# Optimization experiments

Measured on AMD Instinct MI355X. Metric: run time of the kernel, lower is better.

## Reference

```python
import jax, jax.numpy as jnp
import numpy as np

N = 50000       # nodes
E = 800000      # edges
F_IN = 128      # num_node_features
H = 128         # hidden_channels
C = 10          # num_classes
G = 512         # graphs in batch


def _glorot(key, shape):
    fan_in, fan_out = shape
    lim = float(np.sqrt(6.0 / (fan_in + fan_out)))
    return jax.random.uniform(key, shape, jnp.float32, -lim, lim)


def setup_inputs() -> dict:
    key = jax.random.key(0)
    ks = jax.random.split(key, 12)
    x = jax.random.normal(ks[0], (N, F_IN), jnp.float32)
    edge_index = jax.random.randint(ks[1], (2, E), 0, N, dtype=jnp.int32).astype(jnp.int64)
    batch = jnp.sort(jax.random.randint(ks[2], (N,), 0, G, dtype=jnp.int32)).astype(jnp.int64)
    return {
        "x": x,
        "edge_index": edge_index,
        "batch": batch,
        "W1": _glorot(ks[3], (F_IN, H)), "b1": jnp.zeros((H,), jnp.float32),
        "W2": _glorot(ks[4], (H, H)),    "b2": jnp.zeros((H,), jnp.float32),
        "W3": _glorot(ks[5], (H, H)),    "b3": jnp.zeros((H,), jnp.float32),
        "W_lin": _glorot(ks[6], (H, C)), "b_lin": jnp.zeros((C,), jnp.float32),
    }


def _gcn_conv(h_in, W, b, src, dst, dis):
    # GCNConv: D^{-1/2} (A + I) D^{-1/2} (X W) + b  (symmetric norm, self-loops)
    h = h_in @ W                                   # [N, H]
    coef = (dis[src] * dis[dst])[:, None]          # [E, 1]
    msg = h[src] * coef                            # gather + scale
    agg = jax.ops.segment_sum(msg, dst, num_segments=N)  # scatter-add at targets
    agg = agg + h * (dis * dis)[:, None]           # self-loop term
    return agg + b


def reference(x, edge_index, batch, W1, b1, W2, b2, W3, b3, W_lin, b_lin):
    src, dst = edge_index[0], edge_index[1]
    # degree with self-loops (counted at aggregation target, PyG convention)
    deg = jax.ops.segment_sum(jnp.ones((E,), jnp.float32), dst, num_segments=N) + 1.0
    dis = jax.lax.rsqrt(deg)

    h = jax.nn.relu(_gcn_conv(x, W1, b1, src, dst, dis))
    h = jax.nn.relu(_gcn_conv(h, W2, b2, src, dst, dis))
    h = _gcn_conv(h, W3, b3, src, dst, dis)

    # global mean pool over graphs
    counts = jax.ops.segment_sum(jnp.ones((N,), jnp.float32), batch, num_segments=G)
    pooled = jax.ops.segment_sum(h, batch, num_segments=G)
    pooled = pooled / jnp.maximum(counts, 1.0)[:, None]

    # dropout(p=0.5, training=False) -> identity
    return pooled @ W_lin + b_lin
```

## Files before the change

kernel.cpp:

```cpp
#include <hip/hip_runtime.h>

#define NN 50000
#define NE 800000
#define FD 128
#define NG 512
#define NC 10

#define NBUCK 98
#define BSHIFT 9
#define BSTRIDE 10240
#define P1_EPB 4096
#define P1_BLOCKS ((NE + P1_EPB - 1) / P1_EPB)

typedef __attribute__((ext_vector_type(8))) short bf16x8;
typedef __attribute__((ext_vector_type(4))) float f32x4;


__device__ __forceinline__ float bf2f(unsigned short u) {
  return __uint_as_float(((unsigned int)u) << 16);
}
__device__ __forceinline__ unsigned short f2bf(float f) {
  unsigned int b = __float_as_uint(f);
  b += 0x7FFF + ((b >> 16) & 1);
  return (unsigned short)(b >> 16);
}


__global__ __launch_bounds__(128) void init_kernel(int* __restrict__ gcursor) {
  int i = threadIdx.x;
  if (i < NBUCK) gcursor[i] = i * BSTRIDE;
}

__global__ __launch_bounds__(1024) void pass1_kernel(const int* __restrict__ ei,
                                                     int* __restrict__ gcursor,
                                                     unsigned int* __restrict__ bucketBuf) {
  __shared__ unsigned int recs[P1_EPB];
  __shared__ unsigned int grp[P1_EPB];
  __shared__ int bh[NBUCK];
  __shared__ int boff[NBUCK];
  __shared__ int bcur[NBUCK];
  __shared__ int gbase[NBUCK];
  __shared__ int bscan[128];

  int tid = threadIdx.x;
  int e0 = blockIdx.x * P1_EPB;
  int ne = NE - e0; if (ne > P1_EPB) ne = P1_EPB;

  if (tid < NBUCK) bh[tid] = 0;
  __syncthreads();

  for (int i = tid; i < ne; i += 1024) {
    int s = ei[e0 + i];
    int d = ei[NE + e0 + i];
    atomicAdd(&bh[d >> BSHIFT], 1);
    recs[i] = (unsigned int)s | ((unsigned int)d << 16);
  }
  __syncthreads();

  if (tid < 128) bscan[tid] = (tid < NBUCK) ? bh[tid] : 0;
  __syncthreads();
  for (int off = 1; off < 128; off <<= 1) {
    int v = 0;
    if (tid < 128 && tid >= off) v = bscan[tid - off];
    __syncthreads();
    if (tid < 128) bscan[tid] += v;
    __syncthreads();
  }
  if (tid < NBUCK) {
    boff[tid] = bscan[tid] - bh[tid];
    bcur[tid] = bscan[tid] - bh[tid];
    gbase[tid] = (bh[tid] > 0) ? atomicAdd(&gcursor[tid], bh[tid]) : 0;
  }
  __syncthreads();

  for (int i = tid; i < ne; i += 1024) {
    unsigned int r = recs[i];
    int b = (int)(r >> (16 + BSHIFT));
    int p = atomicAdd(&bcur[b], 1);
    grp[p] = r;
  }
  __syncthreads();

  for (int s = tid; s < ne; s += 1024) {
    int lo = 0, hi = NBUCK - 1;
    while (lo < hi) { int m = (lo + hi + 1) >> 1; if (boff[m] <= s) lo = m; else hi = m - 1; }
    bucketBuf[gbase[lo] + (s - boff[lo])] = grp[s];
  }
}

__global__ __launch_bounds__(128) void bucket_scan_kernel(const int* __restrict__ gcur,
                                                          int* __restrict__ bbase) {
  __shared__ int s[128];
  int tid = threadIdx.x;
  int c = (tid < NBUCK) ? (gcur[tid] - tid * BSTRIDE) : 0;
  s[tid] = c;
  __syncthreads();
  for (int off = 1; off < 128; off <<= 1) {
    int v = (tid >= off) ? s[tid - off] : 0;
    __syncthreads();
    s[tid] += v;
    __syncthreads();
  }
  if (tid < NBUCK) bbase[tid] = s[tid] - c;
}

__global__ __launch_bounds__(1024) void pass2_kernel(const unsigned int* __restrict__ bucketBuf,
                                                     const int* __restrict__ gcur,
                                                     const int* __restrict__ bbase,
                                                     int* __restrict__ offs,
                                                     float* __restrict__ dis,
                                                     unsigned short* __restrict__ csr) {
  __shared__ unsigned int raw[BSTRIDE];
  __shared__ unsigned short sorted[BSTRIDE];
  __shared__ int h[512], pos[512], cur[512];

  int b = blockIdx.x;
  int tid = threadIdx.x;
  int nStart = b << BSHIFT;
  int cnt = gcur[b] - b * BSTRIDE;
  if (cnt > BSTRIDE) cnt = BSTRIDE;
  int eStart = bbase[b];

  for (int i = tid; i < cnt; i += 1024) raw[i] = bucketBuf[(size_t)b * BSTRIDE + i];
  if (tid < 512) h[tid] = 0;
  __syncthreads();

  for (int i = tid; i < cnt; i += 1024) atomicAdd(&h[(raw[i] >> 16) - nStart], 1);
  __syncthreads();

  if (tid < 512) pos[tid] = h[tid];
  __syncthreads();
  #pragma unroll
  for (int off = 1; off < 512; off <<= 1) {
    int v = 0;
    if (tid < 512 && tid >= off) v = pos[tid - off];
    __syncthreads();
    if (tid < 512) pos[tid] += v;
    __syncthreads();
  }
  if (tid < 512) {
    int ex = pos[tid] - h[tid];
    cur[tid] = ex;
    int n = nStart + tid;
    if (n < NN) {
      offs[n] = eStart + ex;
      dis[n] = rsqrtf((float)h[tid] + 1.0f);
    }
  }
  if (b == NBUCK - 1 && tid == 0) offs[NN] = eStart + cnt;
  __syncthreads();

  for (int i = tid; i < cnt; i += 1024) {
    unsigned int r = raw[i];
    int d = (int)(r >> 16) - nStart;
    int p = atomicAdd(&cur[d], 1);
    sorted[p] = (unsigned short)(r & 0xFFFFu);
  }
  __syncthreads();

  for (int i = tid; i < cnt; i += 1024) csr[eStart + i] = sorted[i];
}


__global__ __launch_bounds__(256) void prep_w_kernel(const float* __restrict__ W,
                                                     unsigned short* __restrict__ wf) {
  int i = blockIdx.x * 256 + threadIdx.x;
  if (i >= 16384) return;
  int j = i & 7, l = (i >> 3) & 63, ks = (i >> 9) & 3, ct = i >> 11;
  int k = ks * 32 + (l >> 4) * 8 + j;
  int c = ct * 16 + (l & 15);
  float w = W[k * 128 + c];
  unsigned int bb = __float_as_uint(w);
  unsigned int bh = bb & 0xFFFF0000u;
  float r = w - __uint_as_float(bh);
  int base = (((ct * 4 + ks) * 2 + 0) * 64 + l) * 8 + j;
  wf[base] = (unsigned short)(bh >> 16);
  wf[base + 512] = f2bf(r);
}


__global__ __launch_bounds__(256) void gemm_mfma_kernel(const float* __restrict__ A,
                                                        const unsigned short* __restrict__ wf,
                                                        unsigned short* __restrict__ Hb,
                                                        int applyRelu) {
  __shared__ unsigned short ldsW[32768];
  int tid = threadIdx.x;
  {
    const uint4* src = reinterpret_cast<const uint4*>(wf);
    uint4* dst = reinterpret_cast<uint4*>(ldsW);
    #pragma unroll
    for (int i = 0; i < 16; ++i) dst[tid + i * 256] = src[tid + i * 256];
  }
  __syncthreads();

  int w = tid >> 6, lane = tid & 63;
  int rowbase = blockIdx.x * 64 + w * 16;
  int arow = rowbase + (lane & 15);
  if (arow >= NN) arow = 0;
  int kgrp = lane >> 4;

  f32x4 acc[8];
  #pragma unroll
  for (int ct = 0; ct < 8; ++ct) { f32x4 z = {0.f, 0.f, 0.f, 0.f}; acc[ct] = z; }

  #pragma unroll
  for (int ks = 0; ks < 4; ++ks) {
    const float* ap = A + (size_t)arow * FD + ks * 32 + kgrp * 8;
    float4 av0 = *reinterpret_cast<const float4*>(ap);
    float4 av1 = *reinterpret_cast<const float4*>(ap + 4);
    float a[8] = {av0.x, av0.y, av0.z, av0.w, av1.x, av1.y, av1.z, av1.w};
    bf16x8 ahi, alo;
    #pragma unroll
    for (int j = 0; j < 8; ++j) {
      float v = a[j];
      if (applyRelu) v = fmaxf(v, 0.f);
      unsigned int bb = __float_as_uint(v);
      unsigned int bh = bb & 0xFFFF0000u;
      float r = v - __uint_as_float(bh);
      ahi[j] = (short)(bh >> 16);
      alo[j] = (short)f2bf(r);
    }
    #pragma unroll
    for (int ct = 0; ct < 8; ++ct) {
      int off = (((ct * 4 + ks) * 2) * 64 + lane) * 8;
      bf16x8 bhi = *reinterpret_cast<const bf16x8*>(&ldsW[off]);
      bf16x8 blo = *reinterpret_cast<const bf16x8*>(&ldsW[off + 512]);
      acc[ct] = __builtin_amdgcn_mfma_f32_16x16x32_bf16(ahi, bhi, acc[ct], 0, 0, 0);
      acc[ct] = __builtin_amdgcn_mfma_f32_16x16x32_bf16(alo, bhi, acc[ct], 0, 0, 0);
      acc[ct] = __builtin_amdgcn_mfma_f32_16x16x32_bf16(ahi, blo, acc[ct], 0, 0, 0);
    }
  }

  int crow0 = rowbase + kgrp * 4;
  int ccol = lane & 15;
  #pragma unroll
  for (int i = 0; i < 4; ++i) {
    int r = crow0 + i;
    if (r < NN) {
      #pragma unroll
      for (int ct = 0; ct < 8; ++ct) {
        Hb[(size_t)r * FD + ct * 16 + ccol] = f2bf(acc[ct][i]);
      }
    }
  }
}


__global__ __launch_bounds__(256) void agg_edge_kernel(const int* __restrict__ offs,
                                                       const unsigned short* __restrict__ csr,
                                                       const float* __restrict__ dis,
                                                       const unsigned short* __restrict__ Hb,
                                                       const float* __restrict__ b,
                                                       float* __restrict__ AGG) {
  int node = blockIdx.x * 4 + (threadIdx.x >> 6);
  if (node >= NN) return;
  node = __builtin_amdgcn_readfirstlane(node);
  int lane = threadIdx.x & 63;
  int half = lane >> 5;
  int ch = (lane & 31) * 4;
  int beg = offs[node], end = offs[node + 1];
  float disn = dis[node];

  float4 accA, accB = make_float4(0.f, 0.f, 0.f, 0.f);
  {
    float d2 = disn * disn;
    if (half == 0) {
      float4 bb = reinterpret_cast<const float4*>(b)[lane & 31];
      ushort4 hn = *reinterpret_cast<const ushort4*>(&Hb[(size_t)node * FD + ch]);
      accA = make_float4(bb.x + d2 * bf2f(hn.x), bb.y + d2 * bf2f(hn.y),
                         bb.z + d2 * bf2f(hn.z), bb.w + d2 * bf2f(hn.w));
    } else {
      accA = make_float4(0.f, 0.f, 0.f, 0.f);
    }
  }

  int j = beg;
  for (; j + 7 < end; j += 8) {
    int s0 = csr[j + 0 + half];
    int s1 = csr[j + 2 + half];
    int s2 = csr[j + 4 + half];
    int s3 = csr[j + 6 + half];
    float c0 = dis[s0] * disn;
    float c1 = dis[s1] * disn;
    float c2 = dis[s2] * disn;
    float c3 = dis[s3] * disn;
    ushort4 h0 = *reinterpret_cast<const ushort4*>(&Hb[(size_t)s0 * FD + ch]);
    ushort4 h1 = *reinterpret_cast<const ushort4*>(&Hb[(size_t)s1 * FD + ch]);
    ushort4 h2 = *reinterpret_cast<const ushort4*>(&Hb[(size_t)s2 * FD + ch]);
    ushort4 h3 = *reinterpret_cast<const ushort4*>(&Hb[(size_t)s3 * FD + ch]);
    accA.x += c0 * bf2f(h0.x); accA.y += c0 * bf2f(h0.y);
    accA.z += c0 * bf2f(h0.z); accA.w += c0 * bf2f(h0.w);
    accB.x += c1 * bf2f(h1.x); accB.y += c1 * bf2f(h1.y);
    accB.z += c1 * bf2f(h1.z); accB.w += c1 * bf2f(h1.w);
    accA.x += c2 * bf2f(h2.x); accA.y += c2 * bf2f(h2.y);
    accA.z += c2 * bf2f(h2.z); accA.w += c2 * bf2f(h2.w);
    accB.x += c3 * bf2f(h3.x); accB.y += c3 * bf2f(h3.y);
    accB.z += c3 * bf2f(h3.z); accB.w += c3 * bf2f(h3.w);
  }
  for (; j < end; j += 2) {
    int s0 = csr[j];
    float c0 = dis[s0] * disn;
    int s1 = s0; float c1 = 0.f;
    if (j + 1 < end) { s1 = csr[j + 1]; c1 = dis[s1] * disn; }
    int sa = half ? s1 : s0;  float ca = half ? c1 : c0;
    ushort4 ha = *reinterpret_cast<const ushort4*>(&Hb[(size_t)sa * FD + ch]);
    accA.x += ca * bf2f(ha.x); accA.y += ca * bf2f(ha.y);
    accA.z += ca * bf2f(ha.z); accA.w += ca * bf2f(ha.w);
  }
  accA.x += accB.x; accA.y += accB.y; accA.z += accB.z; accA.w += accB.w;

  accA.x += __shfl_xor(accA.x, 32, 64);
  accA.y += __shfl_xor(accA.y, 32, 64);
  accA.z += __shfl_xor(accA.z, 32, 64);
  accA.w += __shfl_xor(accA.w, 32, 64);

  if (half == 0) {
    reinterpret_cast<float4*>(AGG)[(size_t)node * 32 + (lane & 31)] = accA;
  }
}


__device__ __forceinline__ int lower_bound(const int* __restrict__ b, int n, int key) {
  int lo = 0, hi = n;
  while (lo < hi) {
    int m = (lo + hi) >> 1;
    if (b[m] < key) lo = m + 1; else hi = m;
  }
  return lo;
}

__global__ __launch_bounds__(256) void pool_final_kernel(const float* __restrict__ AGG,
                                                         const int* __restrict__ batch,
                                                         const float* __restrict__ Wl,
                                                         const float* __restrict__ bl,
                                                         float* __restrict__ out) {
  int g = blockIdx.x;
  int tid = threadIdx.x;
  int lane = tid & 63, w = tid >> 6;
  int start = lower_bound(batch, NN, g);
  int end = lower_bound(batch, NN, g + 1);

  const float2* AGG2 = reinterpret_cast<const float2*>(AGG);
  float2 acc = make_float2(0.f, 0.f);
  for (int n = start + w; n < end; n += 4) {
    float2 v = AGG2[(size_t)n * 64 + lane];
    acc.x += v.x; acc.y += v.y;
  }
  __shared__ float red[4][FD];
  red[w][lane * 2 + 0] = acc.x;
  red[w][lane * 2 + 1] = acc.y;
  __syncthreads();
  if (w == 0) {
    float px = red[0][lane * 2] + red[1][lane * 2] + red[2][lane * 2] + red[3][lane * 2];
    float py = red[0][lane * 2 + 1] + red[1][lane * 2 + 1] + red[2][lane * 2 + 1] + red[3][lane * 2 + 1];
    float inv = 1.0f / fmaxf((float)(end - start), 1.0f);
    px *= inv; py *= inv;
    float pc[NC];
    #pragma unroll
    for (int c = 0; c < NC; ++c)
      pc[c] = px * Wl[(2 * lane) * NC + c] + py * Wl[(2 * lane + 1) * NC + c];
    #pragma unroll
    for (int off = 32; off > 0; off >>= 1) {
      #pragma unroll
      for (int c = 0; c < NC; ++c) pc[c] += __shfl_down(pc[c], off, 64);
    }
    if (lane == 0) {
      #pragma unroll
      for (int c = 0; c < NC; ++c) out[g * NC + c] = pc[c] + bl[c];
    }
  }
}


extern "C" void kernel_launch(void* const* d_in, const int* in_sizes, int n_in,
                              void* d_out, int out_size, void* d_ws, size_t ws_size,
                              hipStream_t stream) {
  const float* x       = (const float*)d_in[0];
  const int* ei        = (const int*)d_in[1];
  const int* batch     = (const int*)d_in[2];
  const float* W1 = (const float*)d_in[3];
  const float* b1 = (const float*)d_in[4];
  const float* W2 = (const float*)d_in[5];
  const float* b2 = (const float*)d_in[6];
  const float* W3 = (const float*)d_in[7];
  const float* b3 = (const float*)d_in[8];
  const float* Wl = (const float*)d_in[9];
  const float* bl = (const float*)d_in[10];
  float* out = (float*)d_out;

  char* ws = (char*)d_ws;
  size_t o = 0;
  auto alloc = [&](size_t bytes) {
    void* p = ws + o;
    o += bytes;
    o = (o + 255) & ~(size_t)255;
    return p;
  };
  int*   offs   = (int*)  alloc((size_t)(NN + 1) * 4);
  float* dis    = (float*)alloc((size_t)NN * 4);
  int*   gcur   = (int*)  alloc((size_t)NBUCK * 4);
  int*   bbase  = (int*)  alloc((size_t)NBUCK * 4);
  unsigned int* bucketBuf = (unsigned int*)alloc((size_t)NBUCK * BSTRIDE * 4);
  unsigned short* csr = (unsigned short*)alloc((size_t)NE * 2);
  unsigned short* hb  = (unsigned short*)alloc((size_t)NN * FD * 2);
  float* agg    = (float*)alloc((size_t)NN * FD * 4);
  unsigned short* wf1 = (unsigned short*)alloc((size_t)2 * FD * FD * 2);
  unsigned short* wf2 = (unsigned short*)alloc((size_t)2 * FD * FD * 2);
  unsigned short* wf3 = (unsigned short*)alloc((size_t)2 * FD * FD * 2);

  init_kernel<<<1, 128, 0, stream>>>(gcur);
  pass1_kernel<<<P1_BLOCKS, 1024, 0, stream>>>(ei, gcur, bucketBuf);
  bucket_scan_kernel<<<1, 128, 0, stream>>>(gcur, bbase);
  pass2_kernel<<<NBUCK, 1024, 0, stream>>>(bucketBuf, gcur, bbase, offs, dis, csr);
  prep_w_kernel<<<64, 256, 0, stream>>>(W1, wf1);
  prep_w_kernel<<<64, 256, 0, stream>>>(W2, wf2);
  prep_w_kernel<<<64, 256, 0, stream>>>(W3, wf3);

  int gemmGrid = (NN + 63) / 64;
  int nodeGrid = (NN + 3) / 4;

  gemm_mfma_kernel<<<gemmGrid, 256, 0, stream>>>(x, wf1, hb, 0);
  agg_edge_kernel<<<nodeGrid, 256, 0, stream>>>(offs, csr, dis, hb, b1, agg);
  gemm_mfma_kernel<<<gemmGrid, 256, 0, stream>>>(agg, wf2, hb, 1);
  agg_edge_kernel<<<nodeGrid, 256, 0, stream>>>(offs, csr, dis, hb, b2, agg);
  gemm_mfma_kernel<<<gemmGrid, 256, 0, stream>>>(agg, wf3, hb, 1);
  agg_edge_kernel<<<nodeGrid, 256, 0, stream>>>(offs, csr, dis, hb, b3, agg);

  pool_final_kernel<<<NG, 256, 0, stream>>>(agg, batch, Wl, bl, out);
}
```

Before: 205.6 us.

## Double GEMM rows per wave and unify edge aggregation loop with masked tail

The MFMA GEMM kernel now computes 32 rows per wave (128 per block), so each LDS weight fragment load feeds two row tiles and the grid is halved. This cuts LDS traffic per output and interleaves independent MFMA chains, at the cost of more accumulator registers. The edge aggregation kernel drops its scalar tail loop in favour of a single 8-edge loop with clamped indices and zeroed coefficients, and uses four independent accumulators. Tail iterations now do some redundant loads for short neighbour lists.

After: 228.2 us. +11.0%, slower.

```diff
diff --git a/kernel.cpp b/kernel.cpp
--- a/kernel.cpp
+++ b/kernel.cpp
@@ -194,52 +194,82 @@
   __syncthreads();
 
   int w = tid >> 6, lane = tid & 63;
-  int rowbase = blockIdx.x * 64 + w * 16;
-  int arow = rowbase + (lane & 15);
-  if (arow >= NN) arow = 0;
+  int rowbase = blockIdx.x * 128 + w * 32;
   int kgrp = lane >> 4;
-
-  f32x4 acc[8];
+  int r0 = rowbase + (lane & 15);
+  int r1 = r0 + 16;
+  int a0 = (r0 < NN) ? r0 : 0;
+  int a1 = (r1 < NN) ? r1 : 0;
+
+  f32x4 acc0[8], acc1[8];
   #pragma unroll
-  for (int ct = 0; ct < 8; ++ct) { f32x4 z = {0.f, 0.f, 0.f, 0.f}; acc[ct] = z; }
+  for (int ct = 0; ct < 8; ++ct) {
+    f32x4 z = {0.f, 0.f, 0.f, 0.f};
+    acc0[ct] = z; acc1[ct] = z;
+  }
 
   #pragma unroll
   for (int ks = 0; ks < 4; ++ks) {
-    const float* ap = A + (size_t)arow * FD + ks * 32 + kgrp * 8;
-    float4 av0 = *reinterpret_cast<const float4*>(ap);
-    float4 av1 = *reinterpret_cast<const float4*>(ap + 4);
-    float a[8] = {av0.x, av0.y, av0.z, av0.w, av1.x, av1.y, av1.z, av1.w};
-    bf16x8 ahi, alo;
-    #pragma unroll
-    for (int j = 0; j < 8; ++j) {
-      float v = a[j];
-      if (applyRelu) v = fmaxf(v, 0.f);
-      unsigned int bb = __float_as_uint(v);
-      unsigned int bh = bb & 0xFFFF0000u;
-      float r = v - __uint_as_float(bh);
-      ahi[j] = (short)(bh >> 16);
-      alo[j] = (short)f2bf(r);
+    bf16x8 ahi0, alo0, ahi1, alo1;
+    {
+      const float* ap = A + (size_t)a0 * FD + ks * 32 + kgrp * 8;
+      float4 v0 = *reinterpret_cast<const float4*>(ap);
+      float4 v1 = *reinterpret_cast<const float4*>(ap + 4);
+      float a[8] = {v0.x, v0.y, v0.z, v0.w, v1.x, v1.y, v1.z, v1.w};
+      #pragma unroll
+      for (int j = 0; j < 8; ++j) {
+        float v = a[j];
+        if (applyRelu) v = fmaxf(v, 0.f);
+        unsigned int bb = __float_as_uint(v);
+        unsigned int bh = bb & 0xFFFF0000u;
+        float r = v - __uint_as_float(bh);
+        ahi0[j] = (short)(bh >> 16);
+        alo0[j] = (short)f2bf(r);
+      }
+    }
+    {
+      const float* ap = A + (size_t)a1 * FD + ks * 32 + kgrp * 8;
+      float4 v0 = *reinterpret_cast<const float4*>(ap);
+      float4 v1 = *reinterpret_cast<const float4*>(ap + 4);
+      float a[8] = {v0.x, v0.y, v0.z, v0.w, v1.x, v1.y, v1.z, v1.w};
+      #pragma unroll
+      for (int j = 0; j < 8; ++j) {
+        float v = a[j];
+        if (applyRelu) v = fmaxf(v, 0.f);
+        unsigned int bb = __float_as_uint(v);
+        unsigned int bh = bb & 0xFFFF0000u;
+        float r = v - __uint_as_float(bh);
+        ahi1[j] = (short)(bh >> 16);
+        alo1[j] = (short)f2bf(r);
+      }
     }
     #pragma unroll
     for (int ct = 0; ct < 8; ++ct) {
       int off = (((ct * 4 + ks) * 2) * 64 + lane) * 8;
       bf16x8 bhi = *reinterpret_cast<const bf16x8*>(&ldsW[off]);
       bf16x8 blo = *reinterpret_cast<const bf16x8*>(&ldsW[off + 512]);
-      acc[ct] = __builtin_amdgcn_mfma_f32_16x16x32_bf16(ahi, bhi, acc[ct], 0, 0, 0);
-      acc[ct] = __builtin_amdgcn_mfma_f32_16x16x32_bf16(alo, bhi, acc[ct], 0, 0, 0);
-      acc[ct] = __builtin_amdgcn_mfma_f32_16x16x32_bf16(ahi, blo, acc[ct], 0, 0, 0);
-    }
-  }
-
-  int crow0 = rowbase + kgrp * 4;
+      acc0[ct] = __builtin_amdgcn_mfma_f32_16x16x32_bf16(ahi0, bhi, acc0[ct], 0, 0, 0);
+      acc1[ct] = __builtin_amdgcn_mfma_f32_16x16x32_bf16(ahi1, bhi, acc1[ct], 0, 0, 0);
+      acc0[ct] = __builtin_amdgcn_mfma_f32_16x16x32_bf16(alo0, bhi, acc0[ct], 0, 0, 0);
+      acc1[ct] = __builtin_amdgcn_mfma_f32_16x16x32_bf16(alo1, bhi, acc1[ct], 0, 0, 0);
+      acc0[ct] = __builtin_amdgcn_mfma_f32_16x16x32_bf16(ahi0, blo, acc0[ct], 0, 0, 0);
+      acc1[ct] = __builtin_amdgcn_mfma_f32_16x16x32_bf16(ahi1, blo, acc1[ct], 0, 0, 0);
+    }
+  }
+
   int ccol = lane & 15;
   #pragma unroll
-  for (int i = 0; i < 4; ++i) {
-    int r = crow0 + i;
-    if (r < NN) {
-      #pragma unroll
-      for (int ct = 0; ct < 8; ++ct) {
-        Hb[(size_t)r * FD + ct * 16 + ccol] = f2bf(acc[ct][i]);
+  for (int g = 0; g < 2; ++g) {
+    int crow0 = rowbase + g * 16 + kgrp * 4;
+    #pragma unroll
+    for (int i = 0; i < 4; ++i) {
+      int r = crow0 + i;
+      if (r < NN) {
+        #pragma unroll
+        for (int ct = 0; ct < 8; ++ct) {
+          float v = g ? acc1[ct][i] : acc0[ct][i];
+          Hb[(size_t)r * FD + ct * 16 + ccol] = f2bf(v);
+        }
       }
     }
   }
@@ -261,7 +291,9 @@
   int beg = offs[node], end = offs[node + 1];
   float disn = dis[node];
 
-  float4 accA, accB = make_float4(0.f, 0.f, 0.f, 0.f);
+  float4 accA, accB, accC, accD;
+  accB = make_float4(0.f, 0.f, 0.f, 0.f);
+  accC = accB; accD = accB;
   {
     float d2 = disn * disn;
     if (half == 0) {
@@ -274,16 +306,18 @@
     }
   }
 
-  int j = beg;
-  for (; j + 7 < end; j += 8) {
-    int s0 = csr[j + 0 + half];
-    int s1 = csr[j + 2 + half];
-    int s2 = csr[j + 4 + half];
-    int s3 = csr[j + 6 + half];
-    float c0 = dis[s0] * disn;
-    float c1 = dis[s1] * disn;
-    float c2 = dis[s2] * disn;
-    float c3 = dis[s3] * disn;
+  int last = end - 1;
+  for (int j = beg; j < end; j += 8) {
+    int e0 = j + 0 + half, e1 = j + 2 + half, e2 = j + 4 + half, e3 = j + 6 + half;
+    int i0 = (e0 <= last) ? e0 : last;
+    int i1 = (e1 <= last) ? e1 : last;
+    int i2 = (e2 <= last) ? e2 : last;
+    int i3 = (e3 <= last) ? e3 : last;
+    int s0 = csr[i0], s1 = csr[i1], s2 = csr[i2], s3 = csr[i3];
+    float c0 = (e0 <= last) ? dis[s0] * disn : 0.f;
+    float c1 = (e1 <= last) ? dis[s1] * disn : 0.f;
+    float c2 = (e2 <= last) ? dis[s2] * disn : 0.f;
+    float c3 = (e3 <= last) ? dis[s3] * disn : 0.f;
     ushort4 h0 = *reinterpret_cast<const ushort4*>(&Hb[(size_t)s0 * FD + ch]);
     ushort4 h1 = *reinterpret_cast<const ushort4*>(&Hb[(size_t)s1 * FD + ch]);
     ushort4 h2 = *reinterpret_cast<const ushort4*>(&Hb[(size_t)s2 * FD + ch]);
@@ -292,22 +326,15 @@
     accA.z += c0 * bf2f(h0.z); accA.w += c0 * bf2f(h0.w);
     accB.x += c1 * bf2f(h1.x); accB.y += c1 * bf2f(h1.y);
     accB.z += c1 * bf2f(h1.z); accB.w += c1 * bf2f(h1.w);
-    accA.x += c2 * bf2f(h2.x); accA.y += c2 * bf2f(h2.y);
-    accA.z += c2 * bf2f(h2.z); accA.w += c2 * bf2f(h2.w);
-    accB.x += c3 * bf2f(h3.x); accB.y += c3 * bf2f(h3.y);
-    accB.z += c3 * bf2f(h3.z); accB.w += c3 * bf2f(h3.w);
-  }
-  for (; j < end; j += 2) {
-    int s0 = csr[j];
-    float c0 = dis[s0] * disn;
-    int s1 = s0; float c1 = 0.f;
-    if (j + 1 < end) { s1 = csr[j + 1]; c1 = dis[s1] * disn; }
-    int sa = half ? s1 : s0;  float ca = half ? c1 : c0;
-    ushort4 ha = *reinterpret_cast<const ushort4*>(&Hb[(size_t)sa * FD + ch]);
-    accA.x += ca * bf2f(ha.x); accA.y += ca * bf2f(ha.y);
-    accA.z += ca * bf2f(ha.z); accA.w += ca * bf2f(ha.w);
-  }
-  accA.x += accB.x; accA.y += accB.y; accA.z += accB.z; accA.w += accB.w;
+    accC.x += c2 * bf2f(h2.x); accC.y += c2 * bf2f(h2.y);
+    accC.z += c2 * bf2f(h2.z); accC.w += c2 * bf2f(h2.w);
+    accD.x += c3 * bf2f(h3.x); accD.y += c3 * bf2f(h3.y);
+    accD.z += c3 * bf2f(h3.z); accD.w += c3 * bf2f(h3.w);
+  }
+  accA.x += accB.x + accC.x + accD.x;
+  accA.y += accB.y + accC.y + accD.y;
+  accA.z += accB.z + accC.z + accD.z;
+  accA.w += accB.w + accC.w + accD.w;
 
   accA.x += __shfl_xor(accA.x, 32, 64);
   accA.y += __shfl_xor(accA.y, 32, 64);
@@ -416,7 +443,7 @@
   prep_w_kernel<<<64, 256, 0, stream>>>(W2, wf2);
   prep_w_kernel<<<64, 256, 0, stream>>>(W3, wf3);
 
-  int gemmGrid = (NN + 63) / 64;
+  int gemmGrid = (NN + 127) / 128;
   int nodeGrid = (NN + 3) / 4;
 
   gemm_mfma_kernel<<<gemmGrid, 256, 0, stream>>>(x, wf1, hb, 0);
```
